# Optimization experiments

Hardware: AMD Instinct MI355X
Metric: run time of the kernel (lower is better)

## Reference

```python
import jax, jax.numpy as jnp
import numpy as np

MUL = 16            # multiplicity of 0e and 1o in irreps_in/irreps_out
N_NODES = 12500
N_EDGES = 200000
EDGE_ATTR_DIM = 16
WEIGHT_NUMEL = 4 * MUL * MUL  # 4 uvw paths, mul_sh = 1


def setup_inputs() -> dict:
    key = jax.random.key(0)
    ks = jax.random.split(key, 8)
    node_attr = jax.random.normal(ks[0], (N_NODES, 4 * MUL), dtype=jnp.float32)
    edge_index = jax.random.randint(ks[1], (2, N_EDGES), 0, N_NODES, dtype=jnp.int64)
    edge_attr = jax.random.normal(ks[2], (N_EDGES, EDGE_ATTR_DIM), dtype=jnp.float32)
    edge_sh = jax.random.normal(ks[3], (N_EDGES, 4), dtype=jnp.float32)
    # radial ScalarMLP params: Linear(16,16) + SiLU + Linear(16, weight_numel)
    s1 = 1.0 / np.sqrt(EDGE_ATTR_DIM)
    w1 = jax.random.uniform(ks[4], (EDGE_ATTR_DIM, EDGE_ATTR_DIM), jnp.float32, -s1, s1)
    b1 = jax.random.uniform(ks[5], (EDGE_ATTR_DIM,), jnp.float32, -s1, s1)
    w2 = jax.random.uniform(ks[6], (EDGE_ATTR_DIM, WEIGHT_NUMEL), jnp.float32, -s1, s1)
    b2 = jax.random.uniform(ks[7], (WEIGHT_NUMEL,), jnp.float32, -s1, s1)
    return {"node_attr": node_attr, "edge_index": edge_index, "edge_attr": edge_attr,
            "edge_sh": edge_sh, "w1": w1, "b1": b1, "w2": w2, "b2": b2}


def _conv(node_attr, edge_index, edge_attr, edge_sh, w1, b1, w2, b2):
    N = node_attr.shape[0]
    E = edge_attr.shape[0]
    src, dst = edge_index[0], edge_index[1]

    # gather source node features per edge
    x = node_attr[src]                         # [E, 4*MUL]
    x0 = x[:, :MUL]                            # [E, MUL]    (16x0e)
    x1 = x[:, MUL:].reshape(E, MUL, 3)         # [E, MUL, 3] (16x1o)
    y0 = edge_sh[:, 0]                         # [E]   (1x0e)
    y1 = edge_sh[:, 1:4]                       # [E,3] (1x1o)

    # radial MLP -> per-edge tensor-product weights
    h = jax.nn.silu(edge_attr @ w1 + b1)
    W = (h @ w2 + b2).reshape(E, 4, MUL, MUL)  # 4 uvw paths, [E,4,u,w]

    alpha = 1.0 / np.sqrt(2 * MUL).astype(np.float32)  # path norm: 2 paths * MUL fan-in per out irrep
    inv_sqrt3 = np.float32(1.0 / np.sqrt(3.0))

    # path 0: 0e x 0e -> 0e (CG = 1)
    out0 = jnp.einsum('eu,euw->ew', x0 * y0[:, None], W[:, 0])
    # path 1: 1o x 1o -> 0e (CG = delta_ij / sqrt(3), component-normalized)
    out0 = out0 + inv_sqrt3 * jnp.einsum('eui,ei,euw->ew', x1, y1, W[:, 1])
    # path 2: 0e x 1o -> 1o (CG = identity)
    out1 = jnp.einsum('eu,ei,euw->ewi', x0, y1, W[:, 2])
    # path 3: 1o x 0e -> 1o (CG = identity)
    out1 = out1 + jnp.einsum('eui,e,euw->ewi', x1, y0, W[:, 3])

    out_ij = jnp.concatenate([alpha * out0, (alpha * out1).reshape(E, 3 * MUL)], axis=-1)

    # scatter-mean into destination nodes
    sums = jax.ops.segment_sum(out_ij, dst, num_segments=N)
    counts = jax.ops.segment_sum(jnp.ones((E,), out_ij.dtype), dst, num_segments=N)
    return sums / jnp.maximum(counts, 1.0)[:, None]


def reference(node_attr, edge_index, edge_attr, edge_sh, w1, b1, w2, b2):
    return _conv(node_attr, edge_index, edge_attr, edge_sh, w1, b1, w2, b2)
```

## Files before the change

### kernel.cpp

```cpp
#include <hip/hip_runtime.h>
#include <math.h>

#define E_TOTAL  200000
#define NNODES   12500
#define OUT_ELEM 800000
#define NTILE    (E_TOTAL / 64)
#define PAD      64

typedef float    f32x4 __attribute__((ext_vector_type(4)));
typedef _Float16 f16x8 __attribute__((ext_vector_type(8)));
typedef _Float16 f16x4 __attribute__((ext_vector_type(4)));
typedef _Float16 f16x2 __attribute__((ext_vector_type(2)));

union AF { f16x8 f; f16x2 h2[4]; };

static const size_t OFF_CNT    = (size_t)E_TOTAL * 64 * 2;
static const size_t OFF_POS    = OFF_CNT + (size_t)NNODES * 4;
static const size_t OFF_BFRAG  = (OFF_POS + (size_t)NNODES * PAD * 4 + 15) & ~(size_t)15;
static const size_t WS_NEEDED  = OFF_BFRAG + (size_t)36 * 64 * 8 * 2;

__global__ void k_prep(const float* __restrict__ w2, const float* __restrict__ b2,
                       int* __restrict__ cnt, _Float16* __restrict__ bfrag) {
    const int g = blockIdx.x * 256 + threadIdx.x;
    if (g < NNODES) cnt[g] = 0;
    if (g < 36 * 64) {
        const int slot = g >> 6, lane = g & 63;
        const int br = slot / 9, kb = slot - br * 9;
        const int quad = lane >> 4, n = lane & 15;
        const float alpha = 0.17677669529663687f;
        _Float16* dst = bfrag + (size_t)g * 8;
        #pragma unroll
        for (int j = 0; j < 8; ++j) {
            float v;
            if (kb < 8) {
                const int ku = kb * 32 + quad * 8 + j;
                v = w2[(ku >> 4) * 1024 + br * 256 + (ku & 15) * 16 + n];
            } else {
                const int loc = quad * 8 + j;
                v = (loc < 16) ? b2[br * 256 + loc * 16 + n] : 0.0f;
            }
            dst[j] = (_Float16)(alpha * v);
        }
    }
}

__global__ __launch_bounds__(256) void k_conv(
        const float* __restrict__ node_attr,
        const int*   __restrict__ edge_index,
        const float* __restrict__ edge_attr,
        const float* __restrict__ edge_sh,
        const float* __restrict__ w1,
        const float* __restrict__ b1,
        const f16x8* __restrict__ bfrag,
        int* __restrict__ cnt,
        int* __restrict__ pos,
        _Float16* __restrict__ edge_out)
{
    const int t = threadIdx.x;
    __shared__ float  sh_h[64][17];
    __shared__ float4 sh_y[64];
    __shared__ _Float16 sh_s[6][64][24];

    const int ebase = blockIdx.x * 64;
    const float inv_sqrt3 = 0.57735026918962576f;

    if (t < 64) {
        const int e2 = ebase + t;
        const int d = edge_index[E_TOTAL + e2];
        int slot = atomicAdd(&cnt[d], 1);
        if (slot >= PAD) slot = PAD - 1;
        pos[d * PAD + slot] = e2;
    }

    {
        const int e_loc = t & 63, kq = t >> 6;
        const int e = ebase + e_loc;
        const float* ea = edge_attr + (size_t)e * 16;
        float ear[16];
        #pragma unroll
        for (int dq = 0; dq < 4; ++dq) {
            float4 v = *(const float4*)(ea + dq * 4);
            ear[dq * 4 + 0] = v.x; ear[dq * 4 + 1] = v.y;
            ear[dq * 4 + 2] = v.z; ear[dq * 4 + 3] = v.w;
        }
        float4 acc = *(const float4*)(b1 + kq * 4);
        #pragma unroll
        for (int d = 0; d < 16; ++d) {
            float4 wr = *(const float4*)(w1 + d * 16 + kq * 4);
            acc.x += ear[d] * wr.x; acc.y += ear[d] * wr.y;
            acc.z += ear[d] * wr.z; acc.w += ear[d] * wr.w;
        }
        sh_h[e_loc][kq * 4 + 0] = acc.x / (1.0f + __expf(-acc.x));
        sh_h[e_loc][kq * 4 + 1] = acc.y / (1.0f + __expf(-acc.y));
        sh_h[e_loc][kq * 4 + 2] = acc.z / (1.0f + __expf(-acc.z));
        sh_h[e_loc][kq * 4 + 3] = acc.w / (1.0f + __expf(-acc.w));
    }

    {
        const int e_loc = (t & 15) + ((t >> 6) << 4);
        const int pp = (t >> 4) & 3;
        const int u0 = pp * 4;
        const int e = ebase + e_loc;
        const int src = edge_index[e];
        const float4 yv = *(const float4*)(edge_sh + (size_t)e * 4);
        const float* xp = node_attr + (size_t)src * 64;
        float4 x0v = *(const float4*)(xp + u0);
        float x1v[4][3];
        #pragma unroll
        for (int q = 0; q < 4; ++q)
            #pragma unroll
            for (int i = 0; i < 3; ++i)
                x1v[q][i] = xp[16 + (u0 + q) * 3 + i];
        const float* x0p = &x0v.x;
        f16x4 s0h, s1h, x0h, ah, bh, ch;
        #pragma unroll
        for (int q = 0; q < 4; ++q) {
            s0h[q] = (_Float16)(x0p[q] * yv.x);
            s1h[q] = (_Float16)(inv_sqrt3 * (x1v[q][0] * yv.y + x1v[q][1] * yv.z + x1v[q][2] * yv.w));
            x0h[q] = (_Float16)x0p[q];
            ah[q]  = (_Float16)x1v[q][0];
            bh[q]  = (_Float16)x1v[q][1];
            ch[q]  = (_Float16)x1v[q][2];
        }
        *(f16x4*)&sh_s[0][e_loc][u0] = s0h;
        *(f16x4*)&sh_s[1][e_loc][u0] = s1h;
        *(f16x4*)&sh_s[2][e_loc][u0] = x0h;
        *(f16x4*)&sh_s[3][e_loc][u0] = ah;
        *(f16x4*)&sh_s[4][e_loc][u0] = bh;
        *(f16x4*)&sh_s[5][e_loc][u0] = ch;
        if (pp == 0) sh_y[e_loc] = yv;
    }
    __syncthreads();

    const int lane = t & 63, wv = t >> 6;
    const int m = lane & 15, quad = lane >> 4;
    const int e_loc = wv * 16 + m;
    const int qh = quad >> 1, ql = quad & 1;

    AF svh[6];
    #pragma unroll
    for (int b = 0; b < 6; ++b)
        svh[b].f = *(const f16x8*)&sh_s[b][e_loc][ql * 8];
    float hreg[8];
    #pragma unroll
    for (int kb = 0; kb < 8; ++kb) hreg[kb] = sh_h[e_loc][2 * kb + qh];

    f32x4 acc0  = {0.f, 0.f, 0.f, 0.f};
    f32x4 acc2  = {0.f, 0.f, 0.f, 0.f};
    f32x4 acc3a = {0.f, 0.f, 0.f, 0.f};
    f32x4 acc3b = {0.f, 0.f, 0.f, 0.f};
    f32x4 acc3c = {0.f, 0.f, 0.f, 0.f};

    for (int kb = 0; kb < 9; ++kb) {
        const f16x8 B0 = bfrag[(0 * 9 + kb) * 64 + lane];
        const f16x8 B1 = bfrag[(1 * 9 + kb) * 64 + lane];
        const f16x8 B2 = bfrag[(2 * 9 + kb) * 64 + lane];
        const f16x8 B3 = bfrag[(3 * 9 + kb) * 64 + lane];
        const float selF = (kb < 8) ? hreg[kb] : ((quad < 2) ? 1.0f : 0.0f);
        const _Float16 sh1 = (_Float16)selF;
        const f16x2 sel2 = (f16x2){sh1, sh1};
        AF A[6];
        #pragma unroll
        for (int b = 0; b < 6; ++b)
            #pragma unroll
            for (int p = 0; p < 4; ++p)
                A[b].h2[p] = sel2 * svh[b].h2[p];
        acc0  = __builtin_amdgcn_mfma_f32_16x16x32_f16(A[0].f, B0, acc0, 0, 0, 0);
        acc0  = __builtin_amdgcn_mfma_f32_16x16x32_f16(A[1].f, B1, acc0, 0, 0, 0);
        acc2  = __builtin_amdgcn_mfma_f32_16x16x32_f16(A[2].f, B2, acc2, 0, 0, 0);
        acc3a = __builtin_amdgcn_mfma_f32_16x16x32_f16(A[3].f, B3, acc3a, 0, 0, 0);
        acc3b = __builtin_amdgcn_mfma_f32_16x16x32_f16(A[4].f, B3, acc3b, 0, 0, 0);
        acc3c = __builtin_amdgcn_mfma_f32_16x16x32_f16(A[5].f, B3, acc3c, 0, 0, 0);
    }

    #pragma unroll
    for (int r = 0; r < 4; ++r) {
        const int el = wv * 16 + quad * 4 + r;
        const float4 yv = sh_y[el];
        const float t2v = acc2[r];
        const float o0 = acc0[r];
        const float oa = yv.y * t2v + yv.x * acc3a[r];
        const float ob = yv.z * t2v + yv.x * acc3b[r];
        const float oc = yv.w * t2v + yv.x * acc3c[r];
        f16x4 pk = {(_Float16)o0, (_Float16)oa, (_Float16)ob, (_Float16)oc};
        *(f16x4*)(edge_out + (size_t)(ebase + el) * 64 + m * 4) = pk;
    }
}

__global__ __launch_bounds__(256) void k_gather(const _Float16* __restrict__ edge_out,
                                                const int* __restrict__ cnt,
                                                const int* __restrict__ pos,
                                                float* __restrict__ out) {
    const int t = threadIdx.x;
    const int lane = t & 63;
    const int n = blockIdx.x * 4 + (t >> 6);
    int pe;
    if (lane < 16) pe = lane * 4;
    else { const int idx = lane - 16; const int w = idx / 3; pe = w * 4 + 1 + (idx - w * 3); }
    int c = cnt[n];
    if (c > PAD) c = PAD;
    const int p = (lane < c) ? pos[n * PAD + lane] : 0;
    float a0 = 0.f, a1 = 0.f, a2 = 0.f, a3 = 0.f;
    int j = 0;
    for (; j + 4 <= c; j += 4) {
        const int r0 = __shfl(p, j + 0);
        const int r1 = __shfl(p, j + 1);
        const int r2 = __shfl(p, j + 2);
        const int r3 = __shfl(p, j + 3);
        a0 += (float)edge_out[(size_t)r0 * 64 + pe];
        a1 += (float)edge_out[(size_t)r1 * 64 + pe];
        a2 += (float)edge_out[(size_t)r2 * 64 + pe];
        a3 += (float)edge_out[(size_t)r3 * 64 + pe];
    }
    for (; j < c; ++j) {
        const int r = __shfl(p, j);
        a0 += (float)edge_out[(size_t)r * 64 + pe];
    }
    const float acc = (a0 + a1) + (a2 + a3);
    out[n * 64 + lane] = acc / (c > 0 ? (float)c : 1.0f);
}

__global__ void k_zero_f(float* __restrict__ out, float* __restrict__ counts) {
    int i = blockIdx.x * 256 + threadIdx.x;
    if (i < OUT_ELEM) out[i] = 0.0f;
    if (i < NNODES)   counts[i] = 0.0f;
}

#define EPB 80
#define NE  8
__global__ __launch_bounds__(256) void k_conv_atomic(
        const float* __restrict__ node_attr,
        const int*   __restrict__ edge_index,
        const float* __restrict__ edge_attr,
        const float* __restrict__ edge_sh,
        const float* __restrict__ w1,
        const float* __restrict__ b1,
        const float* __restrict__ w2,
        const float* __restrict__ b2,
        float* __restrict__ out,
        float* __restrict__ counts)
{
    const int thr   = threadIdx.x;
    const int lane  = thr & 63;
    const int wv    = thr >> 6;
    const int u     = lane >> 2;
    const int wbase = (lane & 3) * 4;

    float4 w2r[16];
    #pragma unroll
    for (int k = 0; k < 16; ++k)
        w2r[k] = *(const float4*)(w2 + k * 1024 + thr * 4);
    const float4 b2r = *(const float4*)(b2 + thr * 4);

    __shared__ __align__(16) float sh_h[NE][16];
    __shared__ float sh_s0[NE][16];
    __shared__ float sh_s1[NE][16];
    __shared__ float sh_x0[NE][16];
    __shared__ float sh_x1[NE][16][3];
    __shared__ float sh_y0[NE];
    __shared__ float sh_y1[NE][3];
    __shared__ int   sh_dst[NE];

    const float alpha     = 0.17677669529663687f;
    const float inv_sqrt3 = 0.57735026918962576f;
    const int e0 = blockIdx.x * EPB;

    for (int batch = 0; batch < EPB / NE; ++batch) {
        const int ebase = e0 + batch * NE;
        if (thr < 128) {
            const int le = thr >> 4, k = thr & 15;
            const int e = ebase + le;
            float acc = b1[k];
            const float* ea = edge_attr + (size_t)e * 16;
            #pragma unroll
            for (int d = 0; d < 16; ++d) acc += ea[d] * w1[d * 16 + k];
            sh_h[le][k] = acc / (1.0f + __expf(-acc));
            if (k == 0) sh_dst[le] = edge_index[E_TOTAL + e];
        } else {
            const int le = (thr - 128) >> 4, uu = thr & 15;
            const int e = ebase + le;
            const int src = edge_index[e];
            const float y0  = edge_sh[e * 4 + 0];
            const float y1a = edge_sh[e * 4 + 1];
            const float y1b = edge_sh[e * 4 + 2];
            const float y1c = edge_sh[e * 4 + 3];
            const float* xp = node_attr + (size_t)src * 64;
            const float x0v = xp[uu];
            const float xa = xp[16 + uu * 3 + 0];
            const float xb = xp[16 + uu * 3 + 1];
            const float xc = xp[16 + uu * 3 + 2];
            sh_x0[le][uu] = x0v;
            sh_x1[le][uu][0] = xa; sh_x1[le][uu][1] = xb; sh_x1[le][uu][2] = xc;
            sh_s0[le][uu] = x0v * y0;
            sh_s1[le][uu] = inv_sqrt3 * (xa * y1a + xb * y1b + xc * y1c);
            if (uu == 0) {
                sh_y0[le] = y0;
                sh_y1[le][0] = y1a; sh_y1[le][1] = y1b; sh_y1[le][2] = y1c;
            }
        }
        __syncthreads();

        for (int le = 0; le < NE; ++le) {
            float W0 = b2r.x, W1 = b2r.y, W2c = b2r.z, W3c = b2r.w;
            const float4* hv = (const float4*)sh_h[le];
            #pragma unroll
            for (int kk = 0; kk < 4; ++kk) {
                const float4 h4 = hv[kk];
                const int kb = kk * 4;
                W0  += h4.x * w2r[kb + 0].x; W1  += h4.x * w2r[kb + 0].y;
                W2c += h4.x * w2r[kb + 0].z; W3c += h4.x * w2r[kb + 0].w;
                W0  += h4.y * w2r[kb + 1].x; W1  += h4.y * w2r[kb + 1].y;
                W2c += h4.y * w2r[kb + 1].z; W3c += h4.y * w2r[kb + 1].w;
                W0  += h4.z * w2r[kb + 2].x; W1  += h4.z * w2r[kb + 2].y;
                W2c += h4.z * w2r[kb + 2].z; W3c += h4.z * w2r[kb + 2].w;
                W0  += h4.w * w2r[kb + 3].x; W1  += h4.w * w2r[kb + 3].y;
                W2c += h4.w * w2r[kb + 3].z; W3c += h4.w * w2r[kb + 3].w;
            }
            const int dst = sh_dst[le];
            float* op = out + (size_t)dst * 64;
            if (wv == 0 || wv == 1) {
                const float s = (wv == 0) ? sh_s0[le][u] : sh_s1[le][u];
                float v0 = s * W0, v1 = s * W1, v2 = s * W2c, v3 = s * W3c;
                #pragma unroll
                for (int off = 4; off <= 32; off <<= 1) {
                    v0 += __shfl_xor(v0, off); v1 += __shfl_xor(v1, off);
                    v2 += __shfl_xor(v2, off); v3 += __shfl_xor(v3, off);
                }
                if (lane < 4) {
                    atomicAdd(op + wbase + 0, alpha * v0);
                    atomicAdd(op + wbase + 1, alpha * v1);
                    atomicAdd(op + wbase + 2, alpha * v2);
                    atomicAdd(op + wbase + 3, alpha * v3);
                    if (wv == 0 && lane == 0) atomicAdd(&counts[dst], 1.0f);
                }
            } else if (wv == 2) {
                const float s = sh_x0[le][u];
                float v0 = s * W0, v1 = s * W1, v2 = s * W2c, v3 = s * W3c;
                #pragma unroll
                for (int off = 4; off <= 32; off <<= 1) {
                    v0 += __shfl_xor(v0, off); v1 += __shfl_xor(v1, off);
                    v2 += __shfl_xor(v2, off); v3 += __shfl_xor(v3, off);
                }
                if (lane < 4) {
                    const float ya = alpha * sh_y1[le][0];
                    const float yb = alpha * sh_y1[le][1];
                    const float yc = alpha * sh_y1[le][2];
                    float vv[4] = {v0, v1, v2, v3};
                    #pragma unroll
                    for (int q = 0; q < 4; ++q) {
                        float* qp = op + 16 + (wbase + q) * 3;
                        atomicAdd(qp + 0, vv[q] * ya);
                        atomicAdd(qp + 1, vv[q] * yb);
                        atomicAdd(qp + 2, vv[q] * yc);
                    }
                }
            } else {
                const float ay0 = alpha * sh_y0[le];
                #pragma unroll
                for (int i = 0; i < 3; ++i) {
                    const float s = sh_x1[le][u][i];
                    float v0 = s * W0, v1 = s * W1, v2 = s * W2c, v3 = s * W3c;
                    #pragma unroll
                    for (int off = 4; off <= 32; off <<= 1) {
                        v0 += __shfl_xor(v0, off); v1 += __shfl_xor(v1, off);
                        v2 += __shfl_xor(v2, off); v3 += __shfl_xor(v3, off);
                    }
                    if (lane < 4) {
                        atomicAdd(op + 16 + (wbase + 0) * 3 + i, ay0 * v0);
                        atomicAdd(op + 16 + (wbase + 1) * 3 + i, ay0 * v1);
                        atomicAdd(op + 16 + (wbase + 2) * 3 + i, ay0 * v2);
                        atomicAdd(op + 16 + (wbase + 3) * 3 + i, ay0 * v3);
                    }
                }
            }
        }
        __syncthreads();
    }
}

__global__ void k_div(float* __restrict__ out, const float* __restrict__ counts) {
    int i = blockIdx.x * 256 + threadIdx.x;
    if (i < OUT_ELEM) {
        float c = counts[i >> 6];
        out[i] *= 1.0f / fmaxf(c, 1.0f);
    }
}

extern "C" void kernel_launch(void* const* d_in, const int* in_sizes, int n_in,
                              void* d_out, int out_size, void* d_ws, size_t ws_size,
                              hipStream_t stream) {
    const float* node_attr  = (const float*)d_in[0];
    const int*   edge_index = (const int*)d_in[1];
    const float* edge_attr  = (const float*)d_in[2];
    const float* edge_sh    = (const float*)d_in[3];
    const float* w1         = (const float*)d_in[4];
    const float* b1         = (const float*)d_in[5];
    const float* w2         = (const float*)d_in[6];
    const float* b2         = (const float*)d_in[7];
    float* out = (float*)d_out;

    if (ws_size >= WS_NEEDED) {
        char* ws = (char*)d_ws;
        _Float16* edge_out = (_Float16*)ws;
        int*      cnt      = (int*)(ws + OFF_CNT);
        int*      pos      = (int*)(ws + OFF_POS);
        _Float16* bfrag    = (_Float16*)(ws + OFF_BFRAG);

        k_prep<<<(NNODES + 255) / 256, 256, 0, stream>>>(w2, b2, cnt, bfrag);
        k_conv<<<NTILE, 256, 0, stream>>>(
            node_attr, edge_index, edge_attr, edge_sh, w1, b1,
            (const f16x8*)bfrag, cnt, pos, edge_out);
        k_gather<<<NNODES / 4, 256, 0, stream>>>(edge_out, cnt, pos, out);
    } else {
        float* counts = (float*)d_ws;
        k_zero_f<<<(OUT_ELEM + 255) / 256, 256, 0, stream>>>(out, counts);
        k_conv_atomic<<<E_TOTAL / EPB, 256, 0, stream>>>(
            node_attr, edge_index, edge_attr, edge_sh, w1, b1, w2, b2, out, counts);
        k_div<<<(OUT_ELEM + 255) / 256, 256, 0, stream>>>(out, counts);
    }
}
```

Before: 124.2 us.

## Make conv kernel persistent with register prefetch of next tile's inputs

The edge convolution kernel now runs on a fixed grid of 1042 blocks, and each block loops over 64-edge tiles. During the current tile's MFMA work, it prefetches the next tile's edge_attr, edge_sh, gathered node features and destination index into registers. The x1 gather is also vectorised into three float4 loads. This aims to hide global/gather latency behind compute, at the cost of an extra barrier per tile, higher register pressure, and fewer blocks in flight.

Result: slower. 143.2 us (+15.2%).

```diff
diff --git a/kernel.cpp b/kernel.cpp
--- a/kernel.cpp
+++ b/kernel.cpp
@@ -5,6 +5,7 @@
 #define NNODES   12500
 #define OUT_ELEM 800000
 #define NTILE    (E_TOTAL / 64)
+#define GRID_C   1042
 #define PAD      64
 
 typedef float    f32x4 __attribute__((ext_vector_type(4)));
@@ -18,6 +19,13 @@
 static const size_t OFF_POS    = OFF_CNT + (size_t)NNODES * 4;
 static const size_t OFF_BFRAG  = (OFF_POS + (size_t)NNODES * PAD * 4 + 15) & ~(size_t)15;
 static const size_t WS_NEEDED  = OFF_BFRAG + (size_t)36 * 64 * 8 * 2;
+
+struct Pref {
+    float  ear[16];
+    float4 yv, x0v;
+    float  x1f[12];
+    int    dst;
+};
 
 __global__ void k_prep(const float* __restrict__ w2, const float* __restrict__ b2,
                        int* __restrict__ cnt, _Float16* __restrict__ bfrag) {
@@ -61,129 +69,147 @@
     __shared__ float4 sh_y[64];
     __shared__ _Float16 sh_s[6][64][24];
 
-    const int ebase = blockIdx.x * 64;
     const float inv_sqrt3 = 0.57735026918962576f;
-
-    if (t < 64) {
-        const int e2 = ebase + t;
-        const int d = edge_index[E_TOTAL + e2];
-        int slot = atomicAdd(&cnt[d], 1);
-        if (slot >= PAD) slot = PAD - 1;
-        pos[d * PAD + slot] = e2;
-    }
-
-    {
-        const int e_loc = t & 63, kq = t >> 6;
-        const int e = ebase + e_loc;
-        const float* ea = edge_attr + (size_t)e * 16;
-        float ear[16];
-        #pragma unroll
-        for (int dq = 0; dq < 4; ++dq) {
-            float4 v = *(const float4*)(ea + dq * 4);
-            ear[dq * 4 + 0] = v.x; ear[dq * 4 + 1] = v.y;
-            ear[dq * 4 + 2] = v.z; ear[dq * 4 + 3] = v.w;
-        }
-        float4 acc = *(const float4*)(b1 + kq * 4);
-        #pragma unroll
-        for (int d = 0; d < 16; ++d) {
-            float4 wr = *(const float4*)(w1 + d * 16 + kq * 4);
-            acc.x += ear[d] * wr.x; acc.y += ear[d] * wr.y;
-            acc.z += ear[d] * wr.z; acc.w += ear[d] * wr.w;
-        }
-        sh_h[e_loc][kq * 4 + 0] = acc.x / (1.0f + __expf(-acc.x));
-        sh_h[e_loc][kq * 4 + 1] = acc.y / (1.0f + __expf(-acc.y));
-        sh_h[e_loc][kq * 4 + 2] = acc.z / (1.0f + __expf(-acc.z));
-        sh_h[e_loc][kq * 4 + 3] = acc.w / (1.0f + __expf(-acc.w));
-    }
-
-    {
-        const int e_loc = (t & 15) + ((t >> 6) << 4);
-        const int pp = (t >> 4) & 3;
-        const int u0 = pp * 4;
-        const int e = ebase + e_loc;
-        const int src = edge_index[e];
-        const float4 yv = *(const float4*)(edge_sh + (size_t)e * 4);
-        const float* xp = node_attr + (size_t)src * 64;
-        float4 x0v = *(const float4*)(xp + u0);
-        float x1v[4][3];
-        #pragma unroll
-        for (int q = 0; q < 4; ++q)
-            #pragma unroll
-            for (int i = 0; i < 3; ++i)
-                x1v[q][i] = xp[16 + (u0 + q) * 3 + i];
-        const float* x0p = &x0v.x;
-        f16x4 s0h, s1h, x0h, ah, bh, ch;
-        #pragma unroll
-        for (int q = 0; q < 4; ++q) {
-            s0h[q] = (_Float16)(x0p[q] * yv.x);
-            s1h[q] = (_Float16)(inv_sqrt3 * (x1v[q][0] * yv.y + x1v[q][1] * yv.z + x1v[q][2] * yv.w));
-            x0h[q] = (_Float16)x0p[q];
-            ah[q]  = (_Float16)x1v[q][0];
-            bh[q]  = (_Float16)x1v[q][1];
-            ch[q]  = (_Float16)x1v[q][2];
-        }
-        *(f16x4*)&sh_s[0][e_loc][u0] = s0h;
-        *(f16x4*)&sh_s[1][e_loc][u0] = s1h;
-        *(f16x4*)&sh_s[2][e_loc][u0] = x0h;
-        *(f16x4*)&sh_s[3][e_loc][u0] = ah;
-        *(f16x4*)&sh_s[4][e_loc][u0] = bh;
-        *(f16x4*)&sh_s[5][e_loc][u0] = ch;
-        if (pp == 0) sh_y[e_loc] = yv;
-    }
-    __syncthreads();
-
     const int lane = t & 63, wv = t >> 6;
     const int m = lane & 15, quad = lane >> 4;
-    const int e_loc = wv * 16 + m;
+    const int e_loc2 = wv * 16 + m;
     const int qh = quad >> 1, ql = quad & 1;
-
-    AF svh[6];
-    #pragma unroll
-    for (int b = 0; b < 6; ++b)
-        svh[b].f = *(const f16x8*)&sh_s[b][e_loc][ql * 8];
-    float hreg[8];
-    #pragma unroll
-    for (int kb = 0; kb < 8; ++kb) hreg[kb] = sh_h[e_loc][2 * kb + qh];
-
-    f32x4 acc0  = {0.f, 0.f, 0.f, 0.f};
-    f32x4 acc2  = {0.f, 0.f, 0.f, 0.f};
-    f32x4 acc3a = {0.f, 0.f, 0.f, 0.f};
-    f32x4 acc3b = {0.f, 0.f, 0.f, 0.f};
-    f32x4 acc3c = {0.f, 0.f, 0.f, 0.f};
-
-    for (int kb = 0; kb < 9; ++kb) {
-        const f16x8 B0 = bfrag[(0 * 9 + kb) * 64 + lane];
-        const f16x8 B1 = bfrag[(1 * 9 + kb) * 64 + lane];
-        const f16x8 B2 = bfrag[(2 * 9 + kb) * 64 + lane];
-        const f16x8 B3 = bfrag[(3 * 9 + kb) * 64 + lane];
-        const float selF = (kb < 8) ? hreg[kb] : ((quad < 2) ? 1.0f : 0.0f);
-        const _Float16 sh1 = (_Float16)selF;
-        const f16x2 sel2 = (f16x2){sh1, sh1};
-        AF A[6];
+    const int ea_loc = t & 63, kq = t >> 6;
+    const int sb_loc = (t & 15) + ((t >> 6) << 4);
+    const int u0 = ((t >> 4) & 3) * 4;
+
+    Pref P;
+    {
+        const int ebase = blockIdx.x * 64;
+        const float* ea = edge_attr + (size_t)(ebase + ea_loc) * 16;
+        #pragma unroll
+        for (int dq = 0; dq < 4; ++dq)
+            *(float4*)&P.ear[dq * 4] = *(const float4*)(ea + dq * 4);
+        const int e = ebase + sb_loc;
+        const int src = edge_index[e];
+        P.yv  = *(const float4*)(edge_sh + (size_t)e * 4);
+        const float* xp = node_attr + (size_t)src * 64;
+        P.x0v = *(const float4*)(xp + u0);
+        const float* x1p = xp + 16 + u0 * 3;
+        *(float4*)&P.x1f[0] = *(const float4*)(x1p);
+        *(float4*)&P.x1f[4] = *(const float4*)(x1p + 4);
+        *(float4*)&P.x1f[8] = *(const float4*)(x1p + 8);
+        if (t < 64) P.dst = edge_index[E_TOTAL + ebase + t];
+    }
+
+    for (int tile = blockIdx.x; tile < NTILE; tile += gridDim.x) {
+        const int ebase = tile * 64;
+
+        if (t < 64) {
+            int slot = atomicAdd(&cnt[P.dst], 1);
+            if (slot >= PAD) slot = PAD - 1;
+            pos[P.dst * PAD + slot] = ebase + t;
+        }
+        {
+            float4 acc = *(const float4*)(b1 + kq * 4);
+            #pragma unroll
+            for (int d = 0; d < 16; ++d) {
+                float4 wr = *(const float4*)(w1 + d * 16 + kq * 4);
+                acc.x += P.ear[d] * wr.x; acc.y += P.ear[d] * wr.y;
+                acc.z += P.ear[d] * wr.z; acc.w += P.ear[d] * wr.w;
+            }
+            sh_h[ea_loc][kq * 4 + 0] = acc.x / (1.0f + __expf(-acc.x));
+            sh_h[ea_loc][kq * 4 + 1] = acc.y / (1.0f + __expf(-acc.y));
+            sh_h[ea_loc][kq * 4 + 2] = acc.z / (1.0f + __expf(-acc.z));
+            sh_h[ea_loc][kq * 4 + 3] = acc.w / (1.0f + __expf(-acc.w));
+        }
+        {
+            const float* x0p = &P.x0v.x;
+            f16x4 s0h, s1h, x0h, ah, bh, ch;
+            #pragma unroll
+            for (int q = 0; q < 4; ++q) {
+                s0h[q] = (_Float16)(x0p[q] * P.yv.x);
+                s1h[q] = (_Float16)(inv_sqrt3 * (P.x1f[q * 3] * P.yv.y +
+                                                 P.x1f[q * 3 + 1] * P.yv.z +
+                                                 P.x1f[q * 3 + 2] * P.yv.w));
+                x0h[q] = (_Float16)x0p[q];
+                ah[q]  = (_Float16)P.x1f[q * 3 + 0];
+                bh[q]  = (_Float16)P.x1f[q * 3 + 1];
+                ch[q]  = (_Float16)P.x1f[q * 3 + 2];
+            }
+            *(f16x4*)&sh_s[0][sb_loc][u0] = s0h;
+            *(f16x4*)&sh_s[1][sb_loc][u0] = s1h;
+            *(f16x4*)&sh_s[2][sb_loc][u0] = x0h;
+            *(f16x4*)&sh_s[3][sb_loc][u0] = ah;
+            *(f16x4*)&sh_s[4][sb_loc][u0] = bh;
+            *(f16x4*)&sh_s[5][sb_loc][u0] = ch;
+            if (((t >> 4) & 3) == 0) sh_y[sb_loc] = P.yv;
+        }
+        __syncthreads();
+
+        const int ntile = tile + gridDim.x;
+        if (ntile < NTILE) {
+            const int nb = ntile * 64;
+            const float* ea = edge_attr + (size_t)(nb + ea_loc) * 16;
+            #pragma unroll
+            for (int dq = 0; dq < 4; ++dq)
+                *(float4*)&P.ear[dq * 4] = *(const float4*)(ea + dq * 4);
+            const int e = nb + sb_loc;
+            const int src = edge_index[e];
+            P.yv  = *(const float4*)(edge_sh + (size_t)e * 4);
+            const float* xp = node_attr + (size_t)src * 64;
+            P.x0v = *(const float4*)(xp + u0);
+            const float* x1p = xp + 16 + u0 * 3;
+            *(float4*)&P.x1f[0] = *(const float4*)(x1p);
+            *(float4*)&P.x1f[4] = *(const float4*)(x1p + 4);
+            *(float4*)&P.x1f[8] = *(const float4*)(x1p + 8);
+            if (t < 64) P.dst = edge_index[E_TOTAL + nb + t];
+        }
+
+        AF svh[6];
         #pragma unroll
         for (int b = 0; b < 6; ++b)
-            #pragma unroll
-            for (int p = 0; p < 4; ++p)
-                A[b].h2[p] = sel2 * svh[b].h2[p];
-        acc0  = __builtin_amdgcn_mfma_f32_16x16x32_f16(A[0].f, B0, acc0, 0, 0, 0);
-        acc0  = __builtin_amdgcn_mfma_f32_16x16x32_f16(A[1].f, B1, acc0, 0, 0, 0);
-        acc2  = __builtin_amdgcn_mfma_f32_16x16x32_f16(A[2].f, B2, acc2, 0, 0, 0);
-        acc3a = __builtin_amdgcn_mfma_f32_16x16x32_f16(A[3].f, B3, acc3a, 0, 0, 0);
-        acc3b = __builtin_amdgcn_mfma_f32_16x16x32_f16(A[4].f, B3, acc3b, 0, 0, 0);
-        acc3c = __builtin_amdgcn_mfma_f32_16x16x32_f16(A[5].f, B3, acc3c, 0, 0, 0);
-    }
-
-    #pragma unroll
-    for (int r = 0; r < 4; ++r) {
-        const int el = wv * 16 + quad * 4 + r;
-        const float4 yv = sh_y[el];
-        const float t2v = acc2[r];
-        const float o0 = acc0[r];
-        const float oa = yv.y * t2v + yv.x * acc3a[r];
-        const float ob = yv.z * t2v + yv.x * acc3b[r];
-        const float oc = yv.w * t2v + yv.x * acc3c[r];
-        f16x4 pk = {(_Float16)o0, (_Float16)oa, (_Float16)ob, (_Float16)oc};
-        *(f16x4*)(edge_out + (size_t)(ebase + el) * 64 + m * 4) = pk;
+            svh[b].f = *(const f16x8*)&sh_s[b][e_loc2][ql * 8];
+        float hreg[8];
+        #pragma unroll
+        for (int kb = 0; kb < 8; ++kb) hreg[kb] = sh_h[e_loc2][2 * kb + qh];
+
+        f32x4 acc0  = {0.f, 0.f, 0.f, 0.f};
+        f32x4 acc2  = {0.f, 0.f, 0.f, 0.f};
+        f32x4 acc3a = {0.f, 0.f, 0.f, 0.f};
+        f32x4 acc3b = {0.f, 0.f, 0.f, 0.f};
+        f32x4 acc3c = {0.f, 0.f, 0.f, 0.f};
+
+        for (int kb = 0; kb < 9; ++kb) {
+            const f16x8 B0 = bfrag[(0 * 9 + kb) * 64 + lane];
+            const f16x8 B1 = bfrag[(1 * 9 + kb) * 64 + lane];
+            const f16x8 B2 = bfrag[(2 * 9 + kb) * 64 + lane];
+            const f16x8 B3 = bfrag[(3 * 9 + kb) * 64 + lane];
+            const float selF = (kb < 8) ? hreg[kb] : ((quad < 2) ? 1.0f : 0.0f);
+            const _Float16 sh1 = (_Float16)selF;
+            const f16x2 sel2 = (f16x2){sh1, sh1};
+            AF A[6];
+            #pragma unroll
+            for (int b = 0; b < 6; ++b)
+                #pragma unroll
+                for (int p = 0; p < 4; ++p)
+                    A[b].h2[p] = sel2 * svh[b].h2[p];
+            acc0  = __builtin_amdgcn_mfma_f32_16x16x32_f16(A[0].f, B0, acc0, 0, 0, 0);
+            acc0  = __builtin_amdgcn_mfma_f32_16x16x32_f16(A[1].f, B1, acc0, 0, 0, 0);
+            acc2  = __builtin_amdgcn_mfma_f32_16x16x32_f16(A[2].f, B2, acc2, 0, 0, 0);
+            acc3a = __builtin_amdgcn_mfma_f32_16x16x32_f16(A[3].f, B3, acc3a, 0, 0, 0);
+            acc3b = __builtin_amdgcn_mfma_f32_16x16x32_f16(A[4].f, B3, acc3b, 0, 0, 0);
+            acc3c = __builtin_amdgcn_mfma_f32_16x16x32_f16(A[5].f, B3, acc3c, 0, 0, 0);
+        }
+
+        #pragma unroll
+        for (int r = 0; r < 4; ++r) {
+            const int el = wv * 16 + quad * 4 + r;
+            const float4 yv = sh_y[el];
+            const float t2v = acc2[r];
+            const float o0 = acc0[r];
+            const float oa = yv.y * t2v + yv.x * acc3a[r];
+            const float ob = yv.z * t2v + yv.x * acc3b[r];
+            const float oc = yv.w * t2v + yv.x * acc3c[r];
+            f16x4 pk = {(_Float16)o0, (_Float16)oa, (_Float16)ob, (_Float16)oc};
+            *(f16x4*)(edge_out + (size_t)(ebase + el) * 64 + m * 4) = pk;
+        }
+        __syncthreads();
     }
 }
 
@@ -407,7 +433,7 @@
         _Float16* bfrag    = (_Float16*)(ws + OFF_BFRAG);
 
         k_prep<<<(NNODES + 255) / 256, 256, 0, stream>>>(w2, b2, cnt, bfrag);
-        k_conv<<<NTILE, 256, 0, stream>>>(
+        k_conv<<<GRID_C, 256, 0, stream>>>(
             node_attr, edge_index, edge_attr, edge_sh, w1, b1,
             (const f16x8*)bfrag, cnt, pos, edge_out);
         k_gather<<<NNODES / 4, 256, 0, stream>>>(edge_out, cnt, pos, out);
```

## Move radial MLP hidden layer into prep kernel and drop LDS staging in conv

Applied to the files above, without the earlier changes.

The first radial MLP layer (Linear+SiLU) moves into the prep kernel, which now runs over all edge tiles and writes a half-precision hidden buffer laid out so each lane reads its MFMA scale factors with one vector load. The conv kernel stops staging data through shared memory and drops its __syncthreads. Each lane now loads its own node features, edge_sh and hidden values directly from global memory and builds its MFMA A-fragments in registers. This removes the LDS round trip and the barrier, at the cost of an extra kernel pass that writes and reads back a per-edge buffer, plus redundant per-lane global loads.

Measured after the change: 132.1 us. +6.3%, slower.

```diff
diff --git a/kernel.cpp b/kernel.cpp
--- a/kernel.cpp
+++ b/kernel.cpp
@@ -17,10 +17,14 @@
 static const size_t OFF_CNT    = (size_t)E_TOTAL * 64 * 2;
 static const size_t OFF_POS    = OFF_CNT + (size_t)NNODES * 4;
 static const size_t OFF_BFRAG  = (OFF_POS + (size_t)NNODES * PAD * 4 + 15) & ~(size_t)15;
-static const size_t WS_NEEDED  = OFF_BFRAG + (size_t)36 * 64 * 8 * 2;
-
-__global__ void k_prep(const float* __restrict__ w2, const float* __restrict__ b2,
-                       int* __restrict__ cnt, _Float16* __restrict__ bfrag) {
+static const size_t OFF_H16    = OFF_BFRAG + (size_t)36 * 64 * 8 * 2;
+static const size_t WS_NEEDED  = OFF_H16 + (size_t)E_TOTAL * 16 * 2;
+
+__global__ void k_pre(const float* __restrict__ w2, const float* __restrict__ b2,
+                      const float* __restrict__ edge_attr,
+                      const float* __restrict__ w1, const float* __restrict__ b1,
+                      int* __restrict__ cnt, _Float16* __restrict__ bfrag,
+                      _Float16* __restrict__ h16) {
     const int g = blockIdx.x * 256 + threadIdx.x;
     if (g < NNODES) cnt[g] = 0;
     if (g < 36 * 64) {
@@ -42,108 +46,84 @@
             dst[j] = (_Float16)(alpha * v);
         }
     }
+    const int e = g >> 2, kq = g & 3;
+    const float* ea = edge_attr + (size_t)e * 16;
+    float ear[16];
+    #pragma unroll
+    for (int dq = 0; dq < 4; ++dq)
+        *(float4*)&ear[dq * 4] = *(const float4*)(ea + dq * 4);
+    float4 acc = *(const float4*)(b1 + kq * 4);
+    #pragma unroll
+    for (int d = 0; d < 16; ++d) {
+        float4 wr = *(const float4*)(w1 + d * 16 + kq * 4);
+        acc.x += ear[d] * wr.x; acc.y += ear[d] * wr.y;
+        acc.z += ear[d] * wr.z; acc.w += ear[d] * wr.w;
+    }
+    const float h0 = acc.x / (1.0f + __expf(-acc.x));
+    const float h1 = acc.y / (1.0f + __expf(-acc.y));
+    const float h2v = acc.z / (1.0f + __expf(-acc.z));
+    const float h3 = acc.w / (1.0f + __expf(-acc.w));
+    f16x2 ev = {(_Float16)h0, (_Float16)h2v};
+    f16x2 od = {(_Float16)h1, (_Float16)h3};
+    *(f16x2*)(h16 + (size_t)e * 16 + 2 * kq)     = ev;
+    *(f16x2*)(h16 + (size_t)e * 16 + 8 + 2 * kq) = od;
 }
 
 __global__ __launch_bounds__(256) void k_conv(
         const float* __restrict__ node_attr,
         const int*   __restrict__ edge_index,
-        const float* __restrict__ edge_attr,
         const float* __restrict__ edge_sh,
-        const float* __restrict__ w1,
-        const float* __restrict__ b1,
         const f16x8* __restrict__ bfrag,
+        const _Float16* __restrict__ h16,
         int* __restrict__ cnt,
         int* __restrict__ pos,
         _Float16* __restrict__ edge_out)
 {
     const int t = threadIdx.x;
-    __shared__ float  sh_h[64][17];
-    __shared__ float4 sh_y[64];
-    __shared__ _Float16 sh_s[6][64][24];
-
+    const int lane = t & 63, wv = t >> 6;
+    const int m = lane & 15, quad = lane >> 4;
+    const int qh = quad >> 1, ql = quad & 1;
     const int ebase = blockIdx.x * 64;
+    const int e = ebase + wv * 16 + m;
     const float inv_sqrt3 = 0.57735026918962576f;
 
-    if (t < 64) {
-        const int e2 = ebase + t;
-        const int d = edge_index[E_TOTAL + e2];
+    if (quad == 0) {
+        const int d = edge_index[E_TOTAL + e];
         int slot = atomicAdd(&cnt[d], 1);
         if (slot >= PAD) slot = PAD - 1;
-        pos[d * PAD + slot] = e2;
-    }
-
-    {
-        const int e_loc = t & 63, kq = t >> 6;
-        const int e = ebase + e_loc;
-        const float* ea = edge_attr + (size_t)e * 16;
-        float ear[16];
-        #pragma unroll
-        for (int dq = 0; dq < 4; ++dq) {
-            float4 v = *(const float4*)(ea + dq * 4);
-            ear[dq * 4 + 0] = v.x; ear[dq * 4 + 1] = v.y;
-            ear[dq * 4 + 2] = v.z; ear[dq * 4 + 3] = v.w;
-        }
-        float4 acc = *(const float4*)(b1 + kq * 4);
-        #pragma unroll
-        for (int d = 0; d < 16; ++d) {
-            float4 wr = *(const float4*)(w1 + d * 16 + kq * 4);
-            acc.x += ear[d] * wr.x; acc.y += ear[d] * wr.y;
-            acc.z += ear[d] * wr.z; acc.w += ear[d] * wr.w;
-        }
-        sh_h[e_loc][kq * 4 + 0] = acc.x / (1.0f + __expf(-acc.x));
-        sh_h[e_loc][kq * 4 + 1] = acc.y / (1.0f + __expf(-acc.y));
-        sh_h[e_loc][kq * 4 + 2] = acc.z / (1.0f + __expf(-acc.z));
-        sh_h[e_loc][kq * 4 + 3] = acc.w / (1.0f + __expf(-acc.w));
-    }
-
-    {
-        const int e_loc = (t & 15) + ((t >> 6) << 4);
-        const int pp = (t >> 4) & 3;
-        const int u0 = pp * 4;
-        const int e = ebase + e_loc;
-        const int src = edge_index[e];
-        const float4 yv = *(const float4*)(edge_sh + (size_t)e * 4);
-        const float* xp = node_attr + (size_t)src * 64;
-        float4 x0v = *(const float4*)(xp + u0);
-        float x1v[4][3];
-        #pragma unroll
-        for (int q = 0; q < 4; ++q)
-            #pragma unroll
-            for (int i = 0; i < 3; ++i)
-                x1v[q][i] = xp[16 + (u0 + q) * 3 + i];
-        const float* x0p = &x0v.x;
-        f16x4 s0h, s1h, x0h, ah, bh, ch;
-        #pragma unroll
-        for (int q = 0; q < 4; ++q) {
-            s0h[q] = (_Float16)(x0p[q] * yv.x);
-            s1h[q] = (_Float16)(inv_sqrt3 * (x1v[q][0] * yv.y + x1v[q][1] * yv.z + x1v[q][2] * yv.w));
-            x0h[q] = (_Float16)x0p[q];
-            ah[q]  = (_Float16)x1v[q][0];
-            bh[q]  = (_Float16)x1v[q][1];
-            ch[q]  = (_Float16)x1v[q][2];
-        }
-        *(f16x4*)&sh_s[0][e_loc][u0] = s0h;
-        *(f16x4*)&sh_s[1][e_loc][u0] = s1h;
-        *(f16x4*)&sh_s[2][e_loc][u0] = x0h;
-        *(f16x4*)&sh_s[3][e_loc][u0] = ah;
-        *(f16x4*)&sh_s[4][e_loc][u0] = bh;
-        *(f16x4*)&sh_s[5][e_loc][u0] = ch;
-        if (pp == 0) sh_y[e_loc] = yv;
-    }
-    __syncthreads();
-
-    const int lane = t & 63, wv = t >> 6;
-    const int m = lane & 15, quad = lane >> 4;
-    const int e_loc = wv * 16 + m;
-    const int qh = quad >> 1, ql = quad & 1;
+        pos[d * PAD + slot] = e;
+    }
+
+    const int src = edge_index[e];
+    const float4 yv = *(const float4*)(edge_sh + (size_t)e * 4);
+    float4 ye[4];
+    #pragma unroll
+    for (int r = 0; r < 4; ++r)
+        ye[r] = *(const float4*)(edge_sh + (size_t)(ebase + wv * 16 + quad * 4 + r) * 4);
+    const f16x8 hs = *(const f16x8*)(h16 + (size_t)e * 16 + qh * 8);
+    const float* xp = node_attr + (size_t)src * 64;
+    const int u0 = ql * 8;
+    float x0f[8];
+    *(float4*)&x0f[0] = *(const float4*)(xp + u0);
+    *(float4*)&x0f[4] = *(const float4*)(xp + u0 + 4);
+    float x1f[24];
+    #pragma unroll
+    for (int q4 = 0; q4 < 6; ++q4)
+        *(float4*)&x1f[q4 * 4] = *(const float4*)(xp + 16 + u0 * 3 + q4 * 4);
 
     AF svh[6];
     #pragma unroll
-    for (int b = 0; b < 6; ++b)
-        svh[b].f = *(const f16x8*)&sh_s[b][e_loc][ql * 8];
-    float hreg[8];
-    #pragma unroll
-    for (int kb = 0; kb < 8; ++kb) hreg[kb] = sh_h[e_loc][2 * kb + qh];
+    for (int p = 0; p < 4; ++p) {
+        const int q0 = 2 * p, q1 = 2 * p + 1;
+        svh[0].h2[p] = (f16x2){(_Float16)(x0f[q0] * yv.x), (_Float16)(x0f[q1] * yv.x)};
+        svh[1].h2[p] = (f16x2){
+            (_Float16)(inv_sqrt3 * (x1f[q0 * 3] * yv.y + x1f[q0 * 3 + 1] * yv.z + x1f[q0 * 3 + 2] * yv.w)),
+            (_Float16)(inv_sqrt3 * (x1f[q1 * 3] * yv.y + x1f[q1 * 3 + 1] * yv.z + x1f[q1 * 3 + 2] * yv.w))};
+        svh[2].h2[p] = (f16x2){(_Float16)x0f[q0], (_Float16)x0f[q1]};
+        svh[3].h2[p] = (f16x2){(_Float16)x1f[q0 * 3 + 0], (_Float16)x1f[q1 * 3 + 0]};
+        svh[4].h2[p] = (f16x2){(_Float16)x1f[q0 * 3 + 1], (_Float16)x1f[q1 * 3 + 1]};
+        svh[5].h2[p] = (f16x2){(_Float16)x1f[q0 * 3 + 2], (_Float16)x1f[q1 * 3 + 2]};
+    }
 
     f32x4 acc0  = {0.f, 0.f, 0.f, 0.f};
     f32x4 acc2  = {0.f, 0.f, 0.f, 0.f};
@@ -156,9 +136,10 @@
         const f16x8 B1 = bfrag[(1 * 9 + kb) * 64 + lane];
         const f16x8 B2 = bfrag[(2 * 9 + kb) * 64 + lane];
         const f16x8 B3 = bfrag[(3 * 9 + kb) * 64 + lane];
-        const float selF = (kb < 8) ? hreg[kb] : ((quad < 2) ? 1.0f : 0.0f);
-        const _Float16 sh1 = (_Float16)selF;
-        const f16x2 sel2 = (f16x2){sh1, sh1};
+        _Float16 sv;
+        if (kb < 8) sv = hs[kb];
+        else        sv = (quad < 2) ? (_Float16)1.0f : (_Float16)0.0f;
+        const f16x2 sel2 = (f16x2){sv, sv};
         AF A[6];
         #pragma unroll
         for (int b = 0; b < 6; ++b)
@@ -176,12 +157,12 @@
     #pragma unroll
     for (int r = 0; r < 4; ++r) {
         const int el = wv * 16 + quad * 4 + r;
-        const float4 yv = sh_y[el];
+        const float4 yr = ye[r];
         const float t2v = acc2[r];
         const float o0 = acc0[r];
-        const float oa = yv.y * t2v + yv.x * acc3a[r];
-        const float ob = yv.z * t2v + yv.x * acc3b[r];
-        const float oc = yv.w * t2v + yv.x * acc3c[r];
+        const float oa = yr.y * t2v + yr.x * acc3a[r];
+        const float ob = yr.z * t2v + yr.x * acc3b[r];
+        const float oc = yr.w * t2v + yr.x * acc3c[r];
         f16x4 pk = {(_Float16)o0, (_Float16)oa, (_Float16)ob, (_Float16)oc};
         *(f16x4*)(edge_out + (size_t)(ebase + el) * 64 + m * 4) = pk;
     }
@@ -405,11 +386,12 @@
         int*      cnt      = (int*)(ws + OFF_CNT);
         int*      pos      = (int*)(ws + OFF_POS);
         _Float16* bfrag    = (_Float16*)(ws + OFF_BFRAG);
-
-        k_prep<<<(NNODES + 255) / 256, 256, 0, stream>>>(w2, b2, cnt, bfrag);
+        _Float16* h16      = (_Float16*)(ws + OFF_H16);
+
+        k_pre<<<NTILE, 256, 0, stream>>>(w2, b2, edge_attr, w1, b1, cnt, bfrag, h16);
         k_conv<<<NTILE, 256, 0, stream>>>(
-            node_attr, edge_index, edge_attr, edge_sh, w1, b1,
-            (const f16x8*)bfrag, cnt, pos, edge_out);
+            node_attr, edge_index, edge_sh,
+            (const f16x8*)bfrag, h16, cnt, pos, edge_out);
         k_gather<<<NNODES / 4, 256, 0, stream>>>(edge_out, cnt, pos, out);
     } else {
         float* counts = (float*)d_ws;
```
